# Performance work log

Hardware: AMD Instinct MI355X
Metric: run time of the kernel (lower is better)

Reference implementation:

```python
import jax, jax.numpy as jnp
import numpy as np

LMAX = 3
KMAX = [128, 96, 64, 32]   # k_max_l, decreasing in l
N_ATOMS = 10000
N_EDGES = 100000
N_RADIAL = 8
CUTOFF = 5.0

def _bounds(l):
    lo = KMAX[l + 1] if l < LMAX else 0
    return lo, KMAX[l]

def _uncouple(split_list, U):
    # split_list: per l' in 0..L, [n, 2l'+1, k]; U: [3**L, (L+1)**2]
    x = jnp.concatenate(split_list, axis=1)      # [n, (L+1)**2, k]
    return jnp.einsum('dm,nmk->ndk', U, x)       # [n, 3**L, k]

def _couple(f, U, L):
    x = jnp.einsum('dm,ndk->nmk', U, f)          # [n, (L+1)**2, k]
    out, off = [], 0
    for lp in range(L + 1):
        out.append(x[:, off:off + 2 * lp + 1, :])
        off += 2 * lp + 1
    return out

def _forward(r, sh, feat, Wrad, U, Wlin, centers, neighbors):
    # radial basis with smooth cutoff, then per-l channel embedding
    n = jnp.arange(1, N_RADIAL + 1, dtype=r.dtype)
    rb = jnp.sin(n * jnp.pi * r[:, None] / CUTOFF) / (r[:, None] + 1e-6)
    fc = 0.5 * (jnp.cos(jnp.pi * jnp.clip(r / CUTOFF, 0.0, 1.0)) + 1.0)
    rb = rb * fc[:, None]                        # [E, N_RADIAL]
    radial = [rb @ Wrad[l] for l in range(LMAX + 1)]          # [E, KMAX[l]]
    vexp = [sh[l] * radial[l][:, None, :] for l in range(LMAX + 1)]  # [E, 2l+1, KMAX[l]]

    def group(ts, l):
        lo, hi = _bounds(l)
        return [ts[lp][:, :, lo:hi] for lp in range(l + 1)]

    unc_v = [_uncouple(group(vexp, l), U[l]) for l in range(LMAX + 1)]
    unc_f = [_uncouple(group(feat, l), U[l]) for l in range(LMAX + 1)]
    # neighbor gather + elementwise combine in the uncoupled (Cartesian) space
    combined = [unc_v[l] * unc_f[l][neighbors] for l in range(LMAX + 1)]
    # scatter-add pooling over centers (index_add_ equivalent)
    pooled = [jax.ops.segment_sum(c, centers, num_segments=N_ATOMS) for c in combined]
    coupled = [_couple(pooled[l], U[l], l) for l in range(LMAX + 1)]
    cat = [jnp.concatenate([coupled[lp][l] for lp in range(l, LMAX + 1)], axis=-1)
           for l in range(LMAX + 1)]             # [n_atoms, 2l+1, KMAX[l]]
    # NOTE: mp_scaling multiply in the original is dead code (result unused)
    out = [feat[l] + jnp.einsum('nmk,kq->nmq', cat[l], Wlin[l]) for l in range(LMAX + 1)]
    return tuple(out)

def setup_inputs() -> dict:
    key = jax.random.key(0)
    ks = jax.random.split(key, 40)
    inp = {'r': jax.random.uniform(ks[0], (N_EDGES,), minval=0.5, maxval=CUTOFF, dtype=jnp.float32)}
    for l in range(LMAX + 1):
        k = KMAX[l]
        inp[f'sh{l}'] = jax.random.normal(ks[1 + l], (N_EDGES, 2 * l + 1, 1), dtype=jnp.float32)
        inp[f'feat{l}'] = jax.random.normal(ks[5 + l], (N_ATOMS, 2 * l + 1, k), dtype=jnp.float32)
        inp[f'Wrad{l}'] = jax.random.normal(ks[9 + l], (N_RADIAL, k), dtype=jnp.float32) / np.sqrt(N_RADIAL).astype(np.float32)
        inp[f'U{l}'] = jax.random.normal(ks[13 + l], (3 ** l, (l + 1) ** 2), dtype=jnp.float32) / np.float32(np.sqrt((l + 1) ** 2))
        inp[f'Wlin{l}'] = jax.random.normal(ks[17 + l], (k, k), dtype=jnp.float32) / np.sqrt(k).astype(np.float32)
    inp['centers'] = jax.random.randint(ks[21], (N_EDGES,), 0, N_ATOMS, dtype=jnp.int32)
    inp['neighbors'] = jax.random.randint(ks[22], (N_EDGES,), 0, N_ATOMS, dtype=jnp.int32)
    return inp

def reference(r, sh0, sh1, sh2, sh3, feat0, feat1, feat2, feat3,
              Wrad0, Wrad1, Wrad2, Wrad3, U0, U1, U2, U3,
              Wlin0, Wlin1, Wlin2, Wlin3, centers, neighbors):
    return _forward(r, [sh0, sh1, sh2, sh3], [feat0, feat1, feat2, feat3],
                    [Wrad0, Wrad1, Wrad2, Wrad3], [U0, U1, U2, U3],
                    [Wlin0, Wlin1, Wlin2, Wlin3], centers, neighbors)
```

## Files before the change

### kernel.cpp

```cpp
#include <hip/hip_runtime.h>
#include <hip/hip_fp16.h>
#include <math.h>

#define NA 10000
#define NE 100000
#define PI_F 3.14159265358979323846f


__device__ __forceinline__ constexpr int rowC(int row) {
    return (row == 0) ? 0 : (row < 4) ? 1 : (row < 13) ? 2 : 3;
}

__device__ __forceinline__ void stage_U(const float* __restrict__ U0,
                                        const float* __restrict__ U1,
                                        const float* __restrict__ U2,
                                        const float* __restrict__ U3,
                                        float* uLds, int t, int nthr) {
    for (int i = t; i < 526; i += nthr) {
        float v;
        if (i == 0)       v = U0[0];
        else if (i < 13)  v = U1[i - 1];
        else if (i < 94)  v = U2[i - 13];
        else              v = U3[i - 94];
        uLds[i] = v;
    }
}

__global__ __launch_bounds__(256) void kCount(const int* __restrict__ centers,
                                              int* __restrict__ counts)
{
    const int e = blockIdx.x * 256 + threadIdx.x;
    if (e < NE) atomicAdd(&counts[centers[e]], 1);
}

__global__ __launch_bounds__(1024) void kScan(const int* __restrict__ counts,
                                              int* __restrict__ offsets,
                                              int* __restrict__ cursor)
{
    __shared__ int sums[1024];
    const int t = threadIdx.x;
    const int base = t * 10;
    int local[10];
    int s = 0;
#pragma unroll
    for (int j = 0; j < 10; ++j) {
        int idx = base + j;
        int v = (idx < NA) ? counts[idx] : 0;
        local[j] = s;
        s += v;
    }
    sums[t] = s;
    __syncthreads();
    for (int off = 1; off < 1024; off <<= 1) {
        int v = (t >= off) ? sums[t - off] : 0;
        __syncthreads();
        sums[t] += v;
        __syncthreads();
    }
    const int prev = (t == 0) ? 0 : sums[t - 1];
#pragma unroll
    for (int j = 0; j < 10; ++j) {
        int idx = base + j;
        if (idx <= NA) {
            int o = prev + local[j];
            offsets[idx] = o;
            if (idx < NA) cursor[idx] = o;
        }
    }
}

__global__ __launch_bounds__(256) void kPrep(
    const float* __restrict__ f0, const float* __restrict__ f1,
    const float* __restrict__ f2, const float* __restrict__ f3,
    const float* __restrict__ r,
    const float* __restrict__ sh0, const float* __restrict__ sh1,
    const float* __restrict__ sh2, const float* __restrict__ sh3,
    const float* __restrict__ U0, const float* __restrict__ U1,
    const float* __restrict__ U2, const float* __restrict__ U3,
    const int* __restrict__ centers, const int* __restrict__ neighbors,
    int* __restrict__ cursor,
    uint4* __restrict__ uncf16, float* __restrict__ rbbuf,
    float* __restrict__ csbuf, int* __restrict__ nbrs)
{
    __shared__ float uLds[526];
    const int t = threadIdx.x;
    stage_U(U0, U1, U2, U3, uLds, t, 256);
    __syncthreads();

    if (blockIdx.x < 1250) {
        const int la = t >> 5, k = t & 31;
        const int a = blockIdx.x * 8 + la;
        float arr[40];

        {
            arr[0] = uLds[0] * f0[(size_t)a * 128 + 96 + k];
        }
        {
            float x[4];
            x[0] = f0[(size_t)a * 128 + 64 + k];
#pragma unroll
            for (int m = 0; m < 3; ++m) x[1 + m] = f1[(size_t)a * 288 + m * 96 + 64 + k];
#pragma unroll
            for (int d = 0; d < 3; ++d) {
                float acc = 0.f;
#pragma unroll
                for (int m = 0; m < 4; ++m) acc += uLds[1 + d * 4 + m] * x[m];
                arr[1 + d] = acc;
            }
        }
        {
            float x[9];
            x[0] = f0[(size_t)a * 128 + 32 + k];
#pragma unroll
            for (int m = 0; m < 3; ++m) x[1 + m] = f1[(size_t)a * 288 + m * 96 + 32 + k];
#pragma unroll
            for (int m = 0; m < 5; ++m) x[4 + m] = f2[(size_t)a * 320 + m * 64 + 32 + k];
#pragma unroll
            for (int d = 0; d < 9; ++d) {
                float acc = 0.f;
#pragma unroll
                for (int m = 0; m < 9; ++m) acc += uLds[13 + d * 9 + m] * x[m];
                arr[4 + d] = acc;
            }
        }
        {
            float x[16];
            x[0] = f0[(size_t)a * 128 + k];
#pragma unroll
            for (int m = 0; m < 3; ++m) x[1 + m] = f1[(size_t)a * 288 + m * 96 + k];
#pragma unroll
            for (int m = 0; m < 5; ++m) x[4 + m] = f2[(size_t)a * 320 + m * 64 + k];
#pragma unroll
            for (int m = 0; m < 7; ++m) x[9 + m] = f3[(size_t)a * 224 + m * 32 + k];
#pragma unroll
            for (int d = 0; d < 27; ++d) {
                float acc = 0.f;
#pragma unroll
                for (int m = 0; m < 16; ++m) acc += uLds[94 + d * 16 + m] * x[m];
                arr[13 + d] = acc;
            }
        }
        uint4* op = uncf16 + (size_t)a * 160 + k;
#pragma unroll
        for (int jj = 0; jj < 5; ++jj) {
            uint4 w;
            __half2 h0 = __floats2half2_rn(arr[8 * jj + 0], arr[8 * jj + 1]);
            __half2 h1 = __floats2half2_rn(arr[8 * jj + 2], arr[8 * jj + 3]);
            __half2 h2 = __floats2half2_rn(arr[8 * jj + 4], arr[8 * jj + 5]);
            __half2 h3 = __floats2half2_rn(arr[8 * jj + 6], arr[8 * jj + 7]);
            w.x = *(unsigned int*)&h0; w.y = *(unsigned int*)&h1;
            w.z = *(unsigned int*)&h2; w.w = *(unsigned int*)&h3;
            op[jj * 32] = w;
        }
    } else {
        const int e = (blockIdx.x - 1250) * 256 + t;
        if (e >= NE) return;

        const int c_ = centers[e];
        const int pos = atomicAdd(&cursor[c_], 1);
        nbrs[pos] = neighbors[e];

        float shv[16];
        shv[0] = sh0[e];
#pragma unroll
        for (int m = 0; m < 3; ++m) shv[1 + m] = sh1[(size_t)e * 3 + m];
#pragma unroll
        for (int m = 0; m < 5; ++m) shv[4 + m] = sh2[(size_t)e * 5 + m];
#pragma unroll
        for (int m = 0; m < 7; ++m) shv[9 + m] = sh3[(size_t)e * 7 + m];

        const float rv = r[e];
        const float fc = 0.5f * (cosf(PI_F * fminf(rv * 0.2f, 1.0f)) + 1.0f);
        const float pref = fc / (rv + 1e-6f);
        const float step = rv * (PI_F * 0.2f);
        float4 ra, rb;
        ra.x = sinf(1.f * step) * pref; ra.y = sinf(2.f * step) * pref;
        ra.z = sinf(3.f * step) * pref; ra.w = sinf(4.f * step) * pref;
        rb.x = sinf(5.f * step) * pref; rb.y = sinf(6.f * step) * pref;
        rb.z = sinf(7.f * step) * pref; rb.w = sinf(8.f * step) * pref;
        *(float4*)(rbbuf + (size_t)pos * 8)     = ra;
        *(float4*)(rbbuf + (size_t)pos * 8 + 4) = rb;

        const int UO[4] = {0, 1, 13, 94};
        const int RO[4] = {0, 1, 4, 13};
        const int P3[4] = {1, 3, 9, 27};
        float4* cso = (float4*)csbuf + (size_t)pos * 40;
#pragma unroll
        for (int c = 0; c < 4; ++c) {
            const int M2 = (c + 1) * (c + 1);
            for (int d = 0; d < P3[c]; ++d) {
                float4 cv = make_float4(0.f, 0.f, 0.f, 0.f);
                float* cvp = &cv.x;
#pragma unroll
                for (int lp = 0; lp < 4; ++lp) {
                    if (lp > c) break;
                    float s = 0.f;
#pragma unroll
                    for (int ml = 0; ml < 2 * lp + 1; ++ml)
                        s += uLds[UO[c] + d * M2 + lp * lp + ml] * shv[lp * lp + ml];
                    cvp[lp] = s;
                }
                cso[RO[c] + d] = cv;
            }
        }
    }
}

__global__ __launch_bounds__(256, 2) void kB2(
    const float* __restrict__ Wr0, const float* __restrict__ Wr1,
    const float* __restrict__ Wr2, const float* __restrict__ Wr3,
    const int* __restrict__ offsets, const int* __restrict__ nbrs,
    const float* __restrict__ rbbuf, const float* __restrict__ csbuf,
    const uint4* __restrict__ uncf16, float* __restrict__ pooled)
{
    __shared__ float wLds[2560];
    const int t = threadIdx.x;
    for (int i = t; i < 2560; i += 256) {
        float v;
        if (i < 1024)      v = Wr0[i];
        else if (i < 1792) v = Wr1[i - 1024];
        else if (i < 2304) v = Wr2[i - 1792];
        else               v = Wr3[i - 2304];
        wLds[i] = v;
    }
    __syncthreads();

    const int lane = t & 63;
    const int wv = t >> 6;
    const int k = lane & 31;
    const int g2 = lane >> 5;
    const int a = blockIdx.x * 4 + wv;
    const int beg = offsets[a], end = offsets[a + 1];

    float acc[40];
#pragma unroll
    for (int i = 0; i < 40; ++i) acc[i] = 0.f;

    const int KL[4] = {128, 96, 64, 32};
    const int WO[4] = {0, 1024, 1792, 2304};

    int i = beg + g2;
    int nbr = (i < end) ? nbrs[i] : 0;
    for (; i < end; i += 2) {
        const int nbr_nx = (i + 2 < end) ? nbrs[i + 2] : 0;

        const uint4* up = uncf16 + (size_t)nbr * 160 + k;
        const uint4 w0 = up[0 * 32];
        const uint4 w1 = up[1 * 32];
        const uint4 w2 = up[2 * 32];
        const uint4 w3 = up[3 * 32];
        const uint4 w4 = up[4 * 32];

        const float4 r0 = *(const float4*)(rbbuf + (size_t)i * 8);
        const float4 r1 = *(const float4*)(rbbuf + (size_t)i * 8 + 4);
        const float rb[8] = {r0.x, r0.y, r0.z, r0.w, r1.x, r1.y, r1.z, r1.w};

        float rad[4][4];
#pragma unroll
        for (int lp = 0; lp < 4; ++lp) {
#pragma unroll
            for (int c = 0; c < 4; ++c) {
                if (c < lp) continue;
                const int base = 32 * (3 - c);
                float s = 0.f;
#pragma unroll
                for (int n = 0; n < 8; ++n)
                    s += rb[n] * wLds[WO[lp] + n * KL[lp] + base + k];
                rad[lp][c] = s;
            }
        }

        const float4* cs = (const float4*)csbuf + (size_t)i * 40;
        const uint4 ww[5] = {w0, w1, w2, w3, w4};
#pragma unroll
        for (int jj = 0; jj < 5; ++jj) {
            const unsigned int ws[4] = {ww[jj].x, ww[jj].y, ww[jj].z, ww[jj].w};
#pragma unroll
            for (int p2 = 0; p2 < 4; ++p2) {
                const int row0 = 8 * jj + 2 * p2, row1 = row0 + 1;
                const int c0 = rowC(row0), c1 = rowC(row1);
                const __half2 h = *(const __half2*)&ws[p2];
                const float4 cva = cs[row0];
                const float4 cvb = cs[row1];
                float uv0 = cva.x * rad[0][c0];
                if (c0 >= 1) uv0 += cva.y * rad[1][c0];
                if (c0 >= 2) uv0 += cva.z * rad[2][c0];
                if (c0 >= 3) uv0 += cva.w * rad[3][c0];
                float uv1 = cvb.x * rad[0][c1];
                if (c1 >= 1) uv1 += cvb.y * rad[1][c1];
                if (c1 >= 2) uv1 += cvb.z * rad[2][c1];
                if (c1 >= 3) uv1 += cvb.w * rad[3][c1];
                acc[row0] += uv0 * __low2float(h);
                acc[row1] += uv1 * __high2float(h);
            }
        }
        nbr = nbr_nx;
    }

#pragma unroll
    for (int row = 0; row < 40; ++row) acc[row] += __shfl_xor(acc[row], 32);

    float* pp = pooled + (size_t)a * 1280 + k;
#pragma unroll
    for (int rr = 0; rr < 20; ++rr) {
        const float v   = g2 ? acc[rr + 20] : acc[rr];
        const int  row  = g2 ? (rr + 20)    : rr;
        pp[row * 32] = v;
    }
}

__global__ __launch_bounds__(256) void kC_out(
    const float* __restrict__ pooled,
    const float* __restrict__ f0, const float* __restrict__ f1,
    const float* __restrict__ f2, const float* __restrict__ f3,
    const float* __restrict__ U0, const float* __restrict__ U1,
    const float* __restrict__ U2, const float* __restrict__ U3,
    const float* __restrict__ W0, const float* __restrict__ W1,
    const float* __restrict__ W2, const float* __restrict__ W3,
    float* __restrict__ out)
{
    __shared__ float uLds[526];
    __shared__ float plds[4 * 1280];
    __shared__ float clds[120 * 33];
    const int t = threadIdx.x;
    stage_U(U0, U1, U2, U3, uLds, t, 256);
    const int a0 = blockIdx.x * 4;
    {
        const float4* src = (const float4*)(pooled + (size_t)a0 * 1280);
        float4* dst = (float4*)plds;
        for (int i = t; i < 1280; i += 256) dst[i] = src[i];
    }
    __syncthreads();

    if (t < 128) {
        const int la = t >> 5, kk = t & 31;
        clds[(la * 30 + 0) * 33 + kk] = uLds[0] * plds[la * 1280 + 0 * 32 + kk];
    }
#pragma unroll
    for (int s = t; s < 512; s += 256) {
        const int la = s >> 7, rem = s & 127;
        const int m = rem >> 5, kk = rem & 31;
        float acc = 0.f;
#pragma unroll
        for (int d = 0; d < 3; ++d)
            acc += uLds[1 + d * 4 + m] * plds[la * 1280 + (1 + d) * 32 + kk];
        clds[(la * 30 + 1 + m) * 33 + kk] = acc;
    }
    for (int s = t; s < 1152; s += 256) {
        const int la = s / 288, rem = s - la * 288;
        const int m = rem >> 5, kk = rem & 31;
        float acc = 0.f;
#pragma unroll
        for (int d = 0; d < 9; ++d)
            acc += uLds[13 + d * 9 + m] * plds[la * 1280 + (4 + d) * 32 + kk];
        clds[(la * 30 + 5 + m) * 33 + kk] = acc;
    }
    for (int s = t; s < 2048; s += 256) {
        const int la = s >> 9, rem = s & 511;
        const int m = rem >> 5, kk = rem & 31;
        float acc = 0.f;
#pragma unroll
        for (int d = 0; d < 27; ++d)
            acc += uLds[94 + d * 16 + m] * plds[la * 1280 + (13 + d) * 32 + kk];
        clds[(la * 30 + 14 + m) * 33 + kk] = acc;
    }
    __syncthreads();

    int l, m, q;
    bool active = true;
    if (t < 32)       { l = 0; m = 0;                               q = 4 * t; }
    else if (t < 104) { l = 1; int u = t - 32;  m = u / 24; q = 4 * (u % 24); }
    else if (t < 184) { l = 2; int u = t - 104; m = u / 16; q = 4 * (u % 16); }
    else if (t < 240) { l = 3; int u = t - 184; m = u / 8;  q = 4 * (u % 8);  }
    else active = false;

    if (active) {
        const int K  = (l == 0) ? 128 : (l == 1) ? 96 : (l == 2) ? 64 : 32;
        const int MK = (l == 0) ? 128 : (l == 1) ? 288 : (l == 2) ? 320 : 224;
        const size_t Ol = (l == 0) ? 0 : (l == 1) ? 1280000 : (l == 2) ? 4160000 : 7360000;
        const float* F = (l == 0) ? f0 : (l == 1) ? f1 : (l == 2) ? f2 : f3;
        const float* W = (l == 0) ? W0 : (l == 1) ? W1 : (l == 2) ? W2 : W3;
        const int CRB[4] = {0, 1, 5, 14};

        float4 acc[4];
#pragma unroll
        for (int la = 0; la < 4; ++la)
            acc[la] = *(const float4*)(F + (size_t)(a0 + la) * MK + m * K + q);

        for (int j = 0; j < 4 - l; ++j) {
            const int c = l + j;
            const int crow = CRB[c] + l * l + m;
#pragma unroll
            for (int kk = 0; kk < 32; ++kk) {
                const float4 w = *(const float4*)(W + (size_t)(32 * j + kk) * K + q);
#pragma unroll
                for (int la = 0; la < 4; ++la) {
                    const float cv = clds[(la * 30 + crow) * 33 + kk];
                    acc[la].x += cv * w.x; acc[la].y += cv * w.y;
                    acc[la].z += cv * w.z; acc[la].w += cv * w.w;
                }
            }
        }
#pragma unroll
        for (int la = 0; la < 4; ++la)
            *(float4*)(out + Ol + (size_t)(a0 + la) * MK + m * K + q) = acc[la];
    }
}

extern "C" void kernel_launch(void* const* d_in, const int* in_sizes, int n_in,
                              void* d_out, int out_size, void* d_ws, size_t ws_size,
                              hipStream_t stream)
{
    int ir, ish[4], ift[4], iwr[4], iu[4], iwl[4], ic, in_;
    if (in_sizes[2] == 300000) {
        ir = 0;
        for (int l = 0; l < 4; ++l) { ish[l] = 1 + l; ift[l] = 5 + l; iwr[l] = 9 + l; iu[l] = 13 + l; iwl[l] = 17 + l; }
        ic = 21; in_ = 22;
    } else {
        ir = 0;
        for (int l = 0; l < 4; ++l) { ish[l] = 1 + 5 * l; ift[l] = 2 + 5 * l; iwr[l] = 3 + 5 * l; iu[l] = 4 + 5 * l; iwl[l] = 5 + 5 * l; }
        ic = 21; in_ = 22;
    }
    const float* r   = (const float*)d_in[ir];
    const float* sh0 = (const float*)d_in[ish[0]];
    const float* sh1 = (const float*)d_in[ish[1]];
    const float* sh2 = (const float*)d_in[ish[2]];
    const float* sh3 = (const float*)d_in[ish[3]];
    const float* f0  = (const float*)d_in[ift[0]];
    const float* f1  = (const float*)d_in[ift[1]];
    const float* f2  = (const float*)d_in[ift[2]];
    const float* f3  = (const float*)d_in[ift[3]];
    const float* Wr0 = (const float*)d_in[iwr[0]];
    const float* Wr1 = (const float*)d_in[iwr[1]];
    const float* Wr2 = (const float*)d_in[iwr[2]];
    const float* Wr3 = (const float*)d_in[iwr[3]];
    const float* U0  = (const float*)d_in[iu[0]];
    const float* U1  = (const float*)d_in[iu[1]];
    const float* U2  = (const float*)d_in[iu[2]];
    const float* U3  = (const float*)d_in[iu[3]];
    const float* Wl0 = (const float*)d_in[iwl[0]];
    const float* Wl1 = (const float*)d_in[iwl[1]];
    const float* Wl2 = (const float*)d_in[iwl[2]];
    const float* Wl3 = (const float*)d_in[iwl[3]];
    const int* centers   = (const int*)d_in[ic];
    const int* neighbors = (const int*)d_in[in_];

    uint4* uncf16 = (uint4*)d_ws;
    float* pooled = (float*)(uncf16 + (size_t)NA * 160);
    float* rbbuf  = pooled + (size_t)NA * 1280;
    float* csbuf  = rbbuf + (size_t)NE * 8;
    int*   nbrs    = (int*)(csbuf + (size_t)NE * 160);
    int*   counts  = nbrs + NE;
    int*   offsets = counts + NA;
    int*   cursor  = offsets + NA + 1;
    float* outp   = (float*)d_out;

    hipMemsetAsync(counts, 0, NA * sizeof(int), stream);
    kCount<<<(NE + 255) / 256, 256, 0, stream>>>(centers, counts);
    kScan<<<1, 1024, 0, stream>>>(counts, offsets, cursor);
    kPrep<<<1250 + (NE + 255) / 256, 256, 0, stream>>>(
        f0, f1, f2, f3, r, sh0, sh1, sh2, sh3, U0, U1, U2, U3,
        centers, neighbors, cursor, uncf16, rbbuf, csbuf, nbrs);
    kB2<<<NA / 4, 256, 0, stream>>>(Wr0, Wr1, Wr2, Wr3, offsets, nbrs,
                                    rbbuf, csbuf, uncf16, pooled);
    kC_out<<<NA / 4, 256, 0, stream>>>(pooled, f0, f1, f2, f3, U0, U1, U2, U3,
                                       Wl0, Wl1, Wl2, Wl3, outp);
}
```

Baseline: 355.4 us.

## Software-pipeline neighbor feature loads and use sincos recurrence for radial basis

The gather loop now prefetches the next edge's half-precision uncoupled features and radial basis values into registers while the current edge is computed. This overlaps global-memory latency with arithmetic. In the edge-prep kernel, eight sinf calls plus a cosf are replaced by one __sincosf and a Chebyshev recurrence. The cutoff cosine reuses the same cosine value. The prefetch raises register pressure, and the fast sincos with recurrence may change accuracy slightly.

```diff
diff --git a/kernel.cpp b/kernel.cpp
--- a/kernel.cpp
+++ b/kernel.cpp
@@ -170,14 +170,24 @@
         for (int m = 0; m < 7; ++m) shv[9 + m] = sh3[(size_t)e * 7 + m];
 
         const float rv = r[e];
-        const float fc = 0.5f * (cosf(PI_F * fminf(rv * 0.2f, 1.0f)) + 1.0f);
-        const float pref = fc / (rv + 1e-6f);
         const float step = rv * (PI_F * 0.2f);
+        float s1, c1;
+        __sincosf(step, &s1, &c1);
+        const float cfc = (rv < 5.0f) ? c1 : -1.0f;
+        const float pref = (0.5f * (cfc + 1.0f)) / (rv + 1e-6f);
+        const float twoc = 2.0f * c1;
         float4 ra, rb;
-        ra.x = sinf(1.f * step) * pref; ra.y = sinf(2.f * step) * pref;
-        ra.z = sinf(3.f * step) * pref; ra.w = sinf(4.f * step) * pref;
-        rb.x = sinf(5.f * step) * pref; rb.y = sinf(6.f * step) * pref;
-        rb.z = sinf(7.f * step) * pref; rb.w = sinf(8.f * step) * pref;
+        {
+            float sp = s1, spp = 0.0f, s2;
+            ra.x = s1 * pref;
+            s2 = twoc * sp - spp; spp = sp; sp = s2; ra.y = s2 * pref;
+            s2 = twoc * sp - spp; spp = sp; sp = s2; ra.z = s2 * pref;
+            s2 = twoc * sp - spp; spp = sp; sp = s2; ra.w = s2 * pref;
+            s2 = twoc * sp - spp; spp = sp; sp = s2; rb.x = s2 * pref;
+            s2 = twoc * sp - spp; spp = sp; sp = s2; rb.y = s2 * pref;
+            s2 = twoc * sp - spp; spp = sp; sp = s2; rb.z = s2 * pref;
+            s2 = twoc * sp - spp; spp = sp; sp = s2; rb.w = s2 * pref;
+        }
         *(float4*)(rbbuf + (size_t)pos * 8)     = ra;
         *(float4*)(rbbuf + (size_t)pos * 8 + 4) = rb;
 
@@ -240,20 +250,29 @@
     const int WO[4] = {0, 1024, 1792, 2304};
 
     int i = beg + g2;
-    int nbr = (i < end) ? nbrs[i] : 0;
+    uint4 cg0 = make_uint4(0,0,0,0), cg1 = cg0, cg2 = cg0, cg3 = cg0, cg4 = cg0;
+    float4 cr0 = make_float4(0.f,0.f,0.f,0.f), cr1 = cr0;
+    int nbr_nxt = 0;
+    if (i < end) {
+        const int nb = nbrs[i];
+        const uint4* up = uncf16 + (size_t)nb * 160 + k;
+        cg0 = up[0 * 32]; cg1 = up[1 * 32]; cg2 = up[2 * 32];
+        cg3 = up[3 * 32]; cg4 = up[4 * 32];
+        cr0 = *(const float4*)(rbbuf + (size_t)i * 8);
+        cr1 = *(const float4*)(rbbuf + (size_t)i * 8 + 4);
+        nbr_nxt = nbrs[min(i + 2, end - 1)];
+    }
+
     for (; i < end; i += 2) {
-        const int nbr_nx = (i + 2 < end) ? nbrs[i + 2] : 0;
-
-        const uint4* up = uncf16 + (size_t)nbr * 160 + k;
-        const uint4 w0 = up[0 * 32];
-        const uint4 w1 = up[1 * 32];
-        const uint4 w2 = up[2 * 32];
-        const uint4 w3 = up[3 * 32];
-        const uint4 w4 = up[4 * 32];
-
-        const float4 r0 = *(const float4*)(rbbuf + (size_t)i * 8);
-        const float4 r1 = *(const float4*)(rbbuf + (size_t)i * 8 + 4);
-        const float rb[8] = {r0.x, r0.y, r0.z, r0.w, r1.x, r1.y, r1.z, r1.w};
+        const int ip = min(i + 2, end - 1);
+        const uint4* upn = uncf16 + (size_t)nbr_nxt * 160 + k;
+        const uint4 ng0 = upn[0 * 32], ng1 = upn[1 * 32], ng2 = upn[2 * 32];
+        const uint4 ng3 = upn[3 * 32], ng4 = upn[4 * 32];
+        const float4 nr0 = *(const float4*)(rbbuf + (size_t)ip * 8);
+        const float4 nr1 = *(const float4*)(rbbuf + (size_t)ip * 8 + 4);
+        const int nbr_n2 = nbrs[min(i + 4, end - 1)];
+
+        const float rb[8] = {cr0.x, cr0.y, cr0.z, cr0.w, cr1.x, cr1.y, cr1.z, cr1.w};
 
         float rad[4][4];
 #pragma unroll
@@ -271,7 +290,7 @@
         }
 
         const float4* cs = (const float4*)csbuf + (size_t)i * 40;
-        const uint4 ww[5] = {w0, w1, w2, w3, w4};
+        const uint4 ww[5] = {cg0, cg1, cg2, cg3, cg4};
 #pragma unroll
         for (int jj = 0; jj < 5; ++jj) {
             const unsigned int ws[4] = {ww[jj].x, ww[jj].y, ww[jj].z, ww[jj].w};
@@ -294,7 +313,9 @@
                 acc[row1] += uv1 * __high2float(h);
             }
         }
-        nbr = nbr_nx;
+
+        cg0 = ng0; cg1 = ng1; cg2 = ng2; cg3 = ng3; cg4 = ng4;
+        cr0 = nr0; cr1 = nr1; nbr_nxt = nbr_n2;
     }
 
 #pragma unroll
```

New measurement: 472.1 us. 32.8% more time.

## Recompute U·sh coefficients in kB2 from raw sh instead of storing csbuf

Applied to the files above, without the earlier changes.

kPrep now stores only the 16 raw spherical-harmonic values per edge instead of 160 precomputed U·sh coefficients, which cuts the per-edge intermediate buffer write and read traffic by 10x. kB2 stages U in shared memory and each 32-lane group recomputes the coefficients per edge into shared memory, using precomputed per-lane metadata. The radial sines are now built from one __sincosf plus a Chebyshev recurrence, and U staging in kPrep is limited to the atom blocks. The cost is extra LDS traffic and ALU work inside the hot edge loop, with only compiler barriers for intra-wave ordering, plus slightly lower sine accuracy.

```diff
diff --git a/kernel.cpp b/kernel.cpp
--- a/kernel.cpp
+++ b/kernel.cpp
@@ -80,14 +80,15 @@
     const int* __restrict__ centers, const int* __restrict__ neighbors,
     int* __restrict__ cursor,
     uint4* __restrict__ uncf16, float* __restrict__ rbbuf,
-    float* __restrict__ csbuf, int* __restrict__ nbrs)
+    float* __restrict__ shbuf, int* __restrict__ nbrs)
 {
-    __shared__ float uLds[526];
     const int t = threadIdx.x;
-    stage_U(U0, U1, U2, U3, uLds, t, 256);
-    __syncthreads();
 
     if (blockIdx.x < 1250) {
+        __shared__ float uLds[526];
+        stage_U(U0, U1, U2, U3, uLds, t, 256);
+        __syncthreads();
+
         const int la = t >> 5, k = t & 31;
         const int a = blockIdx.x * 8 + la;
         float arr[40];
@@ -170,50 +171,48 @@
         for (int m = 0; m < 7; ++m) shv[9 + m] = sh3[(size_t)e * 7 + m];
 
         const float rv = r[e];
-        const float fc = 0.5f * (cosf(PI_F * fminf(rv * 0.2f, 1.0f)) + 1.0f);
-        const float pref = fc / (rv + 1e-6f);
         const float step = rv * (PI_F * 0.2f);
+        float s1, c1;
+        __sincosf(step, &s1, &c1);
+        const float cfc = (rv < 5.0f) ? c1 : -1.0f;
+        const float pref = (0.5f * (cfc + 1.0f)) / (rv + 1e-6f);
+        const float twoc = 2.0f * c1;
         float4 ra, rb;
-        ra.x = sinf(1.f * step) * pref; ra.y = sinf(2.f * step) * pref;
-        ra.z = sinf(3.f * step) * pref; ra.w = sinf(4.f * step) * pref;
-        rb.x = sinf(5.f * step) * pref; rb.y = sinf(6.f * step) * pref;
-        rb.z = sinf(7.f * step) * pref; rb.w = sinf(8.f * step) * pref;
+        {
+            float sp = s1, spp = 0.0f, s2;
+            ra.x = s1 * pref;
+            s2 = twoc * sp - spp; spp = sp; sp = s2; ra.y = s2 * pref;
+            s2 = twoc * sp - spp; spp = sp; sp = s2; ra.z = s2 * pref;
+            s2 = twoc * sp - spp; spp = sp; sp = s2; ra.w = s2 * pref;
+            s2 = twoc * sp - spp; spp = sp; sp = s2; rb.x = s2 * pref;
+            s2 = twoc * sp - spp; spp = sp; sp = s2; rb.y = s2 * pref;
+            s2 = twoc * sp - spp; spp = sp; sp = s2; rb.z = s2 * pref;
+            s2 = twoc * sp - spp; spp = sp; sp = s2; rb.w = s2 * pref;
+        }
         *(float4*)(rbbuf + (size_t)pos * 8)     = ra;
         *(float4*)(rbbuf + (size_t)pos * 8 + 4) = rb;
 
-        const int UO[4] = {0, 1, 13, 94};
-        const int RO[4] = {0, 1, 4, 13};
-        const int P3[4] = {1, 3, 9, 27};
-        float4* cso = (float4*)csbuf + (size_t)pos * 40;
-#pragma unroll
-        for (int c = 0; c < 4; ++c) {
-            const int M2 = (c + 1) * (c + 1);
-            for (int d = 0; d < P3[c]; ++d) {
-                float4 cv = make_float4(0.f, 0.f, 0.f, 0.f);
-                float* cvp = &cv.x;
-#pragma unroll
-                for (int lp = 0; lp < 4; ++lp) {
-                    if (lp > c) break;
-                    float s = 0.f;
-#pragma unroll
-                    for (int ml = 0; ml < 2 * lp + 1; ++ml)
-                        s += uLds[UO[c] + d * M2 + lp * lp + ml] * shv[lp * lp + ml];
-                    cvp[lp] = s;
-                }
-                cso[RO[c] + d] = cv;
-            }
-        }
+        float4* so = (float4*)(shbuf + (size_t)pos * 16);
+        so[0] = make_float4(shv[0],  shv[1],  shv[2],  shv[3]);
+        so[1] = make_float4(shv[4],  shv[5],  shv[6],  shv[7]);
+        so[2] = make_float4(shv[8],  shv[9],  shv[10], shv[11]);
+        so[3] = make_float4(shv[12], shv[13], shv[14], shv[15]);
     }
 }
 
 __global__ __launch_bounds__(256, 2) void kB2(
     const float* __restrict__ Wr0, const float* __restrict__ Wr1,
     const float* __restrict__ Wr2, const float* __restrict__ Wr3,
+    const float* __restrict__ U0, const float* __restrict__ U1,
+    const float* __restrict__ U2, const float* __restrict__ U3,
     const int* __restrict__ offsets, const int* __restrict__ nbrs,
-    const float* __restrict__ rbbuf, const float* __restrict__ csbuf,
+    const float* __restrict__ rbbuf, const float* __restrict__ shbuf,
     const uint4* __restrict__ uncf16, float* __restrict__ pooled)
 {
     __shared__ float wLds[2560];
+    __shared__ float uLds[526];
+    __shared__ float shLds[8 * 16];
+    __shared__ float csLds[8 * 160];
     const int t = threadIdx.x;
     for (int i = t; i < 2560; i += 256) {
         float v;
@@ -223,14 +222,29 @@
         else               v = Wr3[i - 2304];
         wLds[i] = v;
     }
+    stage_U(U0, U1, U2, U3, uLds, t, 256);
     __syncthreads();
 
     const int lane = t & 63;
     const int wv = t >> 6;
     const int k = lane & 31;
     const int g2 = lane >> 5;
+    const int grp = t >> 5;
+    const int shb = grp * 16, csb = grp * 160;
     const int a = blockIdx.x * 4 + wv;
     const int beg = offsets[a], end = offsets[a + 1];
+
+    unsigned int mmeta[5];
+#pragma unroll
+    for (int s = 0; s < 5; ++s) {
+        const int v = k + 32 * s;
+        int row, lp, uoff;
+        if (v == 0)      { row = 0; lp = 0; uoff = 0; }
+        else if (v < 7)  { const int u = v - 1;  const int d = u >> 1; lp = u & 1;     row = 1 + d;  uoff = 1  + d * 4  + lp * lp; }
+        else if (v < 34) { const int u = v - 7;  const int d = u / 3;  lp = u - 3 * d; row = 4 + d;  uoff = 13 + d * 9  + lp * lp; }
+        else             { const int u = v - 34; const int d = u >> 2; lp = u & 3;     row = 13 + d; uoff = 94 + d * 16 + lp * lp; }
+        mmeta[s] = (unsigned int)row | ((unsigned int)lp << 8) | ((unsigned int)uoff << 16);
+    }
 
     float acc[40];
 #pragma unroll
@@ -253,6 +267,10 @@
 
         const float4 r0 = *(const float4*)(rbbuf + (size_t)i * 8);
         const float4 r1 = *(const float4*)(rbbuf + (size_t)i * 8 + 4);
+
+        if (k < 16) shLds[shb + k] = shbuf[(size_t)i * 16 + k];
+        asm volatile("" ::: "memory");
+
         const float rb[8] = {r0.x, r0.y, r0.z, r0.w, r1.x, r1.y, r1.z, r1.w};
 
         float rad[4][4];
@@ -270,7 +288,22 @@
             }
         }
 
-        const float4* cs = (const float4*)csbuf + (size_t)i * 40;
+#pragma unroll
+        for (int s = 0; s < 5; ++s) {
+            if (s < 4 || k < 14) {
+                const unsigned int mm = mmeta[s];
+                const int row  = (int)(mm & 255u);
+                const int lp   = (int)((mm >> 8) & 255u);
+                const int uoff = (int)(mm >> 16);
+                const int lp2  = lp * lp;
+                float a_ = uLds[uoff] * shLds[shb + lp2];
+                for (int ml = 1; ml < 2 * lp + 1; ++ml)
+                    a_ += uLds[uoff + ml] * shLds[shb + lp2 + ml];
+                csLds[csb + row * 4 + lp] = a_;
+            }
+        }
+        asm volatile("" ::: "memory");
+
         const uint4 ww[5] = {w0, w1, w2, w3, w4};
 #pragma unroll
         for (int jj = 0; jj < 5; ++jj) {
@@ -280,8 +313,8 @@
                 const int row0 = 8 * jj + 2 * p2, row1 = row0 + 1;
                 const int c0 = rowC(row0), c1 = rowC(row1);
                 const __half2 h = *(const __half2*)&ws[p2];
-                const float4 cva = cs[row0];
-                const float4 cvb = cs[row1];
+                const float4 cva = *(const float4*)&csLds[csb + row0 * 4];
+                const float4 cvb = *(const float4*)&csLds[csb + row1 * 4];
                 float uv0 = cva.x * rad[0][c0];
                 if (c0 >= 1) uv0 += cva.y * rad[1][c0];
                 if (c0 >= 2) uv0 += cva.z * rad[2][c0];
@@ -448,8 +481,8 @@
     uint4* uncf16 = (uint4*)d_ws;
     float* pooled = (float*)(uncf16 + (size_t)NA * 160);
     float* rbbuf  = pooled + (size_t)NA * 1280;
-    float* csbuf  = rbbuf + (size_t)NE * 8;
-    int*   nbrs    = (int*)(csbuf + (size_t)NE * 160);
+    float* shbuf  = rbbuf + (size_t)NE * 8;
+    int*   nbrs    = (int*)(shbuf + (size_t)NE * 16);
     int*   counts  = nbrs + NE;
     int*   offsets = counts + NA;
     int*   cursor  = offsets + NA + 1;
@@ -460,9 +493,9 @@
     kScan<<<1, 1024, 0, stream>>>(counts, offsets, cursor);
     kPrep<<<1250 + (NE + 255) / 256, 256, 0, stream>>>(
         f0, f1, f2, f3, r, sh0, sh1, sh2, sh3, U0, U1, U2, U3,
-        centers, neighbors, cursor, uncf16, rbbuf, csbuf, nbrs);
-    kB2<<<NA / 4, 256, 0, stream>>>(Wr0, Wr1, Wr2, Wr3, offsets, nbrs,
-                                    rbbuf, csbuf, uncf16, pooled);
+        centers, neighbors, cursor, uncf16, rbbuf, shbuf, nbrs);
+    kB2<<<NA / 4, 256, 0, stream>>>(Wr0, Wr1, Wr2, Wr3, U0, U1, U2, U3,
+                                    offsets, nbrs, rbbuf, shbuf, uncf16, pooled);
     kC_out<<<NA / 4, 256, 0, stream>>>(pooled, f0, f1, f2, f3, U0, U1, U2, U3,
                                        Wl0, Wl1, Wl2, Wl3, outp);
 }
```

Measured after the change: 381.9 us. 1.07x slower.

## Use persistent atomic work queue in kB2 and Chebyshev recurrence for radial sines

Applied to the files above, without the earlier changes.

kB2 becomes a persistent kernel with 1024 blocks: each wave pulls atom indices from a global atomic counter instead of one wave per fixed atom. This is meant to balance the uneven neighbor counts per atom and avoid launching 2500 blocks that each stage the radial weights into LDS. Separately, kPrep computes the eight radial sines from one __sincosf call plus the Chebyshev recurrence sin((n+1)x)=2cos(x)sin(nx)-sin((n-1)x), and reuses cos(x) for the cutoff, replacing nine transcendental calls. The recurrence and the fast intrinsic can differ slightly in accuracy, and the queue counter is zeroed by extending the existing memset.

```diff
diff --git a/kernel.cpp b/kernel.cpp
--- a/kernel.cpp
+++ b/kernel.cpp
@@ -170,14 +170,24 @@
         for (int m = 0; m < 7; ++m) shv[9 + m] = sh3[(size_t)e * 7 + m];
 
         const float rv = r[e];
-        const float fc = 0.5f * (cosf(PI_F * fminf(rv * 0.2f, 1.0f)) + 1.0f);
-        const float pref = fc / (rv + 1e-6f);
         const float step = rv * (PI_F * 0.2f);
+        float s1, c1;
+        __sincosf(step, &s1, &c1);
+        const float cfc = (rv < 5.0f) ? c1 : -1.0f;
+        const float pref = (0.5f * (cfc + 1.0f)) / (rv + 1e-6f);
+        const float twoc = 2.0f * c1;
         float4 ra, rb;
-        ra.x = sinf(1.f * step) * pref; ra.y = sinf(2.f * step) * pref;
-        ra.z = sinf(3.f * step) * pref; ra.w = sinf(4.f * step) * pref;
-        rb.x = sinf(5.f * step) * pref; rb.y = sinf(6.f * step) * pref;
-        rb.z = sinf(7.f * step) * pref; rb.w = sinf(8.f * step) * pref;
+        {
+            float sp = s1, spp = 0.0f, s2;
+            ra.x = s1 * pref;
+            s2 = twoc * sp - spp; spp = sp; sp = s2; ra.y = s2 * pref;
+            s2 = twoc * sp - spp; spp = sp; sp = s2; ra.z = s2 * pref;
+            s2 = twoc * sp - spp; spp = sp; sp = s2; ra.w = s2 * pref;
+            s2 = twoc * sp - spp; spp = sp; sp = s2; rb.x = s2 * pref;
+            s2 = twoc * sp - spp; spp = sp; sp = s2; rb.y = s2 * pref;
+            s2 = twoc * sp - spp; spp = sp; sp = s2; rb.z = s2 * pref;
+            s2 = twoc * sp - spp; spp = sp; sp = s2; rb.w = s2 * pref;
+        }
         *(float4*)(rbbuf + (size_t)pos * 8)     = ra;
         *(float4*)(rbbuf + (size_t)pos * 8 + 4) = rb;
 
@@ -211,7 +221,8 @@
     const float* __restrict__ Wr2, const float* __restrict__ Wr3,
     const int* __restrict__ offsets, const int* __restrict__ nbrs,
     const float* __restrict__ rbbuf, const float* __restrict__ csbuf,
-    const uint4* __restrict__ uncf16, float* __restrict__ pooled)
+    const uint4* __restrict__ uncf16, int* __restrict__ qcur,
+    float* __restrict__ pooled)
 {
     __shared__ float wLds[2560];
     const int t = threadIdx.x;
@@ -226,86 +237,92 @@
     __syncthreads();
 
     const int lane = t & 63;
-    const int wv = t >> 6;
     const int k = lane & 31;
     const int g2 = lane >> 5;
-    const int a = blockIdx.x * 4 + wv;
-    const int beg = offsets[a], end = offsets[a + 1];
-
-    float acc[40];
-#pragma unroll
-    for (int i = 0; i < 40; ++i) acc[i] = 0.f;
 
     const int KL[4] = {128, 96, 64, 32};
     const int WO[4] = {0, 1024, 1792, 2304};
 
-    int i = beg + g2;
-    int nbr = (i < end) ? nbrs[i] : 0;
-    for (; i < end; i += 2) {
-        const int nbr_nx = (i + 2 < end) ? nbrs[i + 2] : 0;
-
-        const uint4* up = uncf16 + (size_t)nbr * 160 + k;
-        const uint4 w0 = up[0 * 32];
-        const uint4 w1 = up[1 * 32];
-        const uint4 w2 = up[2 * 32];
-        const uint4 w3 = up[3 * 32];
-        const uint4 w4 = up[4 * 32];
-
-        const float4 r0 = *(const float4*)(rbbuf + (size_t)i * 8);
-        const float4 r1 = *(const float4*)(rbbuf + (size_t)i * 8 + 4);
-        const float rb[8] = {r0.x, r0.y, r0.z, r0.w, r1.x, r1.y, r1.z, r1.w};
-
-        float rad[4][4];
-#pragma unroll
-        for (int lp = 0; lp < 4; ++lp) {
-#pragma unroll
-            for (int c = 0; c < 4; ++c) {
-                if (c < lp) continue;
-                const int base = 32 * (3 - c);
-                float s = 0.f;
-#pragma unroll
-                for (int n = 0; n < 8; ++n)
-                    s += rb[n] * wLds[WO[lp] + n * KL[lp] + base + k];
-                rad[lp][c] = s;
-            }
-        }
-
-        const float4* cs = (const float4*)csbuf + (size_t)i * 40;
-        const uint4 ww[5] = {w0, w1, w2, w3, w4};
-#pragma unroll
-        for (int jj = 0; jj < 5; ++jj) {
-            const unsigned int ws[4] = {ww[jj].x, ww[jj].y, ww[jj].z, ww[jj].w};
-#pragma unroll
-            for (int p2 = 0; p2 < 4; ++p2) {
-                const int row0 = 8 * jj + 2 * p2, row1 = row0 + 1;
-                const int c0 = rowC(row0), c1 = rowC(row1);
-                const __half2 h = *(const __half2*)&ws[p2];
-                const float4 cva = cs[row0];
-                const float4 cvb = cs[row1];
-                float uv0 = cva.x * rad[0][c0];
-                if (c0 >= 1) uv0 += cva.y * rad[1][c0];
-                if (c0 >= 2) uv0 += cva.z * rad[2][c0];
-                if (c0 >= 3) uv0 += cva.w * rad[3][c0];
-                float uv1 = cvb.x * rad[0][c1];
-                if (c1 >= 1) uv1 += cvb.y * rad[1][c1];
-                if (c1 >= 2) uv1 += cvb.z * rad[2][c1];
-                if (c1 >= 3) uv1 += cvb.w * rad[3][c1];
-                acc[row0] += uv0 * __low2float(h);
-                acc[row1] += uv1 * __high2float(h);
-            }
-        }
-        nbr = nbr_nx;
-    }
-
-#pragma unroll
-    for (int row = 0; row < 40; ++row) acc[row] += __shfl_xor(acc[row], 32);
-
-    float* pp = pooled + (size_t)a * 1280 + k;
-#pragma unroll
-    for (int rr = 0; rr < 20; ++rr) {
-        const float v   = g2 ? acc[rr + 20] : acc[rr];
-        const int  row  = g2 ? (rr + 20)    : rr;
-        pp[row * 32] = v;
+    for (;;) {
+        int a;
+        if (lane == 0) a = atomicAdd(qcur, 1);
+        a = __shfl(a, 0);
+        if (a >= NA) break;
+
+        const int beg = offsets[a], end = offsets[a + 1];
+
+        float acc[40];
+#pragma unroll
+        for (int i = 0; i < 40; ++i) acc[i] = 0.f;
+
+        int i = beg + g2;
+        int nbr = (i < end) ? nbrs[i] : 0;
+        for (; i < end; i += 2) {
+            const int nbr_nx = (i + 2 < end) ? nbrs[i + 2] : 0;
+
+            const uint4* up = uncf16 + (size_t)nbr * 160 + k;
+            const uint4 w0 = up[0 * 32];
+            const uint4 w1 = up[1 * 32];
+            const uint4 w2 = up[2 * 32];
+            const uint4 w3 = up[3 * 32];
+            const uint4 w4 = up[4 * 32];
+
+            const float4 r0 = *(const float4*)(rbbuf + (size_t)i * 8);
+            const float4 r1 = *(const float4*)(rbbuf + (size_t)i * 8 + 4);
+            const float rb[8] = {r0.x, r0.y, r0.z, r0.w, r1.x, r1.y, r1.z, r1.w};
+
+            float rad[4][4];
+#pragma unroll
+            for (int lp = 0; lp < 4; ++lp) {
+#pragma unroll
+                for (int c = 0; c < 4; ++c) {
+                    if (c < lp) continue;
+                    const int base = 32 * (3 - c);
+                    float s = 0.f;
+#pragma unroll
+                    for (int n = 0; n < 8; ++n)
+                        s += rb[n] * wLds[WO[lp] + n * KL[lp] + base + k];
+                    rad[lp][c] = s;
+                }
+            }
+
+            const float4* cs = (const float4*)csbuf + (size_t)i * 40;
+            const uint4 ww[5] = {w0, w1, w2, w3, w4};
+#pragma unroll
+            for (int jj = 0; jj < 5; ++jj) {
+                const unsigned int ws[4] = {ww[jj].x, ww[jj].y, ww[jj].z, ww[jj].w};
+#pragma unroll
+                for (int p2 = 0; p2 < 4; ++p2) {
+                    const int row0 = 8 * jj + 2 * p2, row1 = row0 + 1;
+                    const int c0 = rowC(row0), c1 = rowC(row1);
+                    const __half2 h = *(const __half2*)&ws[p2];
+                    const float4 cva = cs[row0];
+                    const float4 cvb = cs[row1];
+                    float uv0 = cva.x * rad[0][c0];
+                    if (c0 >= 1) uv0 += cva.y * rad[1][c0];
+                    if (c0 >= 2) uv0 += cva.z * rad[2][c0];
+                    if (c0 >= 3) uv0 += cva.w * rad[3][c0];
+                    float uv1 = cvb.x * rad[0][c1];
+                    if (c1 >= 1) uv1 += cvb.y * rad[1][c1];
+                    if (c1 >= 2) uv1 += cvb.z * rad[2][c1];
+                    if (c1 >= 3) uv1 += cvb.w * rad[3][c1];
+                    acc[row0] += uv0 * __low2float(h);
+                    acc[row1] += uv1 * __high2float(h);
+                }
+            }
+            nbr = nbr_nx;
+        }
+
+#pragma unroll
+        for (int row = 0; row < 40; ++row) acc[row] += __shfl_xor(acc[row], 32);
+
+        float* pp = pooled + (size_t)a * 1280 + k;
+#pragma unroll
+        for (int rr = 0; rr < 20; ++rr) {
+            const float v   = g2 ? acc[rr + 20] : acc[rr];
+            const int  row  = g2 ? (rr + 20)    : rr;
+            pp[row * 32] = v;
+        }
     }
 }
 
@@ -451,18 +468,19 @@
     float* csbuf  = rbbuf + (size_t)NE * 8;
     int*   nbrs    = (int*)(csbuf + (size_t)NE * 160);
     int*   counts  = nbrs + NE;
-    int*   offsets = counts + NA;
+    int*   qcur    = counts + NA;
+    int*   offsets = qcur + 1;
     int*   cursor  = offsets + NA + 1;
     float* outp   = (float*)d_out;
 
-    hipMemsetAsync(counts, 0, NA * sizeof(int), stream);
+    hipMemsetAsync(counts, 0, (NA + 1) * sizeof(int), stream);
     kCount<<<(NE + 255) / 256, 256, 0, stream>>>(centers, counts);
     kScan<<<1, 1024, 0, stream>>>(counts, offsets, cursor);
     kPrep<<<1250 + (NE + 255) / 256, 256, 0, stream>>>(
         f0, f1, f2, f3, r, sh0, sh1, sh2, sh3, U0, U1, U2, U3,
         centers, neighbors, cursor, uncf16, rbbuf, csbuf, nbrs);
-    kB2<<<NA / 4, 256, 0, stream>>>(Wr0, Wr1, Wr2, Wr3, offsets, nbrs,
-                                    rbbuf, csbuf, uncf16, pooled);
+    kB2<<<1024, 256, 0, stream>>>(Wr0, Wr1, Wr2, Wr3, offsets, nbrs,
+                                  rbbuf, csbuf, uncf16, qcur, pooled);
     kC_out<<<NA / 4, 256, 0, stream>>>(pooled, f0, f1, f2, f3, U0, U1, U2, U3,
                                        Wl0, Wl1, Wl2, Wl3, outp);
 }
```

Measured after the change: 462.9 us. 1.3x slower.
